# Kernel tuning notes

Measured on AMD Instinct MI355X. Metric: run time of the kernel, lower is better.

The kernel has to match this reference:

```python
import jax, jax.numpy as jnp
import numpy as np
from jax.scipy.special import digamma, gammaln

NUM_CLASSES = 3
FOCAL_GAMMA = 2.0
LABEL_SMOOTHING = 0.1
EVIDENTIAL_W = 0.1
CONTRASTIVE_W = 0.1
BOUNDARY_W = 0.15
TRIPLET_W = 0.1
QUALITY_W = 0.1
TRIPLET_MARGIN = 1.5


def setup_inputs() -> dict:
    key = jax.random.key(0)
    k1, k2, k3 = jax.random.split(key, 3)
    B, D = 4096, 512
    logits = jax.random.normal(k1, (B, NUM_CLASSES), dtype=jnp.float32)
    targets = jax.random.randint(k2, (B,), 0, 3)
    features = jax.random.normal(k3, (B, D), dtype=jnp.float32)
    alpha = jax.random.uniform(jax.random.fold_in(key, 7), (B, NUM_CLASSES), dtype=jnp.float32)
    focal_alpha = jnp.array([1.0, 2.0, 1.5], dtype=jnp.float32)
    class_weights = jnp.array([1.0, 2.0, 1.5], dtype=jnp.float32)
    return {"logits": logits, "targets": targets, "features": features,
            "alpha": alpha, "epoch": 1, "focal_alpha": focal_alpha,
            "class_weights": class_weights}


def reference(logits, targets, features, alpha, epoch, focal_alpha, class_weights):
    B = logits.shape[0]
    C = NUM_CLASSES

    # ---- focal loss (label-smoothed CE, torch semantics) ----
    logp = jax.nn.log_softmax(logits, axis=1)                      # [B,C]
    nll = -jnp.take_along_axis(logp, targets[:, None], axis=1)[:, 0]
    ce_ls = (1.0 - LABEL_SMOOTHING) * nll + LABEL_SMOOTHING * (-logp.mean(axis=1))
    pt = jnp.exp(-ce_ls)
    focal = (focal_alpha[targets] * (1.0 - pt) ** FOCAL_GAMMA * ce_ls).mean()

    # ---- weighted CE (torch weighted mean: sum(w*nll)/sum(w)) ----
    w = class_weights[targets]
    ce = (w * nll).sum() / w.sum()

    # ---- enhanced boundary loss ----
    probs = jax.nn.softmax(logits, axis=1)
    real = targets == 0
    semi = targets == 1
    syn = targets == 2
    rb = jnp.where(real, probs[:, 1] + 0.6 * probs[:, 2], 0.0).sum()
    sb = jnp.where(syn, probs[:, 1] + 0.4 * probs[:, 0], 0.0).sum()
    mb = jnp.where(semi, 1.0 - probs[:, 1] + 0.3 * (probs[:, 0] + probs[:, 2]), 0.0).sum()
    boundary = (rb + sb + 4.5 * mb) / (B + 1e-8)

    total = 0.4 * focal + 0.3 * ce + BOUNDARY_W * boundary

    # ---- normalized features and pairwise cosine-sim matrix ----
    norms = jnp.linalg.norm(features, axis=1, keepdims=True)
    f = features / jnp.maximum(norms, 1e-12)
    sim = f @ f.T                                                  # [B,B]
    same = targets[:, None] == targets[None, :]
    eye = jnp.eye(B, dtype=bool)

    # ---- enhanced contrastive loss ----
    pos = jnp.where(same, (1.0 - sim) ** 2, 0.0).sum()
    neg = jnp.where(~same, jnp.clip(sim - 0.2, 0.0) ** 2, 0.0).sum()
    semi_pair = semi[:, None] & semi[None, :]
    semi_l = jnp.where(semi_pair, (1.0 - sim) ** 2, 0.0).sum()
    contrastive = (pos + neg + 4.0 * semi_l) / (B * B + 1e-8)

    # ---- enhanced triplet loss (batch-hard, vectorized) ----
    d2 = jnp.clip(2.0 - 2.0 * sim, 0.0)
    dist = jnp.sqrt(jnp.where(eye, 1.0, d2))  # diag masked; safe sqrt
    pos_mask = same & ~eye
    neg_mask = ~same
    hp = jnp.max(jnp.where(pos_mask, dist, -jnp.inf), axis=1)
    hn = jnp.min(jnp.where(neg_mask, dist, jnp.inf), axis=1)
    valid = pos_mask.any(axis=1) & neg_mask.any(axis=1)
    margin = TRIPLET_MARGIN * jnp.where(targets == 1, 2.5, 1.0)
    tl = jax.nn.relu(hp - hn + margin)
    cnt = valid.sum()
    triplet = jnp.where(cnt > 0,
                        jnp.where(valid, tl, 0.0).sum() / jnp.maximum(cnt, 1),
                        0.0)

    # ---- quality-invariant loss (upper-tri same-class pairs) ----
    upper = jnp.triu(jnp.ones((B, B), dtype=bool), k=1)
    qmask = same & upper
    npairs = qmask.sum()
    q = jnp.where(qmask, (1.0 - sim) ** 2, 0.0).sum() / jnp.maximum(npairs, 1)
    frac2 = syn.astype(jnp.float32).mean()
    q = q * jnp.where(syn.sum() > 0, 1.0 + 2.5 * frac2, 1.0)
    quality = jnp.where(npairs > 0, q, 0.0)

    # ---- evidential loss ----
    onehot = jax.nn.one_hot(targets, C, dtype=jnp.float32)
    S = alpha.sum(axis=1, keepdims=True) + 1e-8
    likelihood = (onehot * (digamma(S) - digamma(alpha + 1e-8))).sum(axis=1)
    at = onehot + (1.0 - onehot) * alpha
    ats = at.sum(axis=1) + 1e-8
    kl = (gammaln(ats) - gammaln(at + 1e-8).sum(axis=1)
          + ((at - 1.0) * (digamma(at + 1e-8) - digamma(ats[:, None] + 1e-8))).sum(axis=1))
    annealing = min(1.0, (epoch / 25.0) ** 2)
    evidential = likelihood.mean() + annealing * 0.2 * kl.mean()

    total = (total + CONTRASTIVE_W * contrastive + TRIPLET_W * triplet
             + QUALITY_W * quality + EVIDENTIAL_W * evidential)
    return total
```

## Files before the change

kernel.cpp:

```cpp
#include <hip/hip_runtime.h>
#include <hip/hip_bf16.h>
#include <cstdint>

typedef __attribute__((ext_vector_type(8))) __bf16 bf8;
typedef __attribute__((ext_vector_type(4))) float f32x4;

#if defined(__has_builtin)
#if __has_builtin(__builtin_amdgcn_global_load_lds)
#define USE_GLL 1
#endif
#endif
#ifndef USE_GLL
#define USE_GLL 0
#endif

#if USE_GLL
__device__ __forceinline__ void gll16(const __bf16* g, __bf16* l){
  __builtin_amdgcn_global_load_lds(
      (const __attribute__((address_space(1))) void*)g,
      (__attribute__((address_space(3))) void*)l, 16, 0, 0);
}
#endif

__device__ __forceinline__ unsigned mapf(float x){
  unsigned u = __float_as_uint(x);
  return (u & 0x80000000u) ? ~u : (u | 0x80000000u);
}
__device__ __forceinline__ float unmapf(unsigned u){
  return __uint_as_float((u & 0x80000000u) ? (u & 0x7FFFFFFFu) : ~u);
}

__device__ float digammaf_(float x){
  float r = 0.f;
  while (x < 6.f){ r -= 1.f/x; x += 1.f; }
  float inv = 1.f/x, inv2 = inv*inv;
  r += logf(x) - 0.5f*inv
     - inv2*(0.08333333333f - inv2*(0.008333333333f - inv2*0.003968253968f));
  return r;
}

__global__ __launch_bounds__(256) void k_prep(const float* __restrict__ feat,
    __bf16* __restrict__ fb2,
    const float* __restrict__ logits, const int* __restrict__ targets,
    const float* __restrict__ alpha,  const float* __restrict__ fa,
    const float* __restrict__ cw, int B, int D,
    float* __restrict__ psum, unsigned* rowMinU, unsigned* rowMaxU){
  int bid = blockIdx.x, tid = threadIdx.x;
  int wave = tid >> 6, lane = tid & 63;

  int row = bid*4 + wave;
  const float* src = feat + (size_t)row*D;
  float ss = 0.f;
  for (int c = lane*4; c < D; c += 64*4){
    float4 v = *(const float4*)(src + c);
    ss += v.x*v.x + v.y*v.y + v.z*v.z + v.w*v.w;
  }
  #pragma unroll
  for (int off=32; off; off>>=1) ss += __shfl_xor(ss, off);
  float inv = 1.f / fmaxf(sqrtf(ss), 1e-12f);

  int p = row >> 6, r = row & 63;
  int rsw = (r >> 1) & 3;
  int NCH = D >> 5;
  for (int c = lane*8; c < D; c += 64*8){
    float4 v0 = *(const float4*)(src + c);
    float4 v1 = *(const float4*)(src + c + 4);
    bf8 o;
    o[0]=(__bf16)(v0.x*inv); o[1]=(__bf16)(v0.y*inv);
    o[2]=(__bf16)(v0.z*inv); o[3]=(__bf16)(v0.w*inv);
    o[4]=(__bf16)(v1.x*inv); o[5]=(__bf16)(v1.y*inv);
    o[6]=(__bf16)(v1.z*inv); o[7]=(__bf16)(v1.w*inv);
    int cc = c >> 5;
    int cb = (c >> 3) & 3;
    size_t off = (size_t)(p*NCH + cc)*2048 + r*32 + ((cb ^ rsw)*8);
    *(bf8*)(fb2 + off) = o;
  }

  if (tid < 4){ rowMinU[bid*4+tid] = 0xFFFFFFFFu; rowMaxU[bid*4+tid] = 0u; }

  if (wave == 0){
    float r0=0.f,r1=0.f,r2=0.f,r3=0.f,r4=0.f,r5=0.f;
    if (lane < 4){
      int i = bid*4 + lane;
      float l0=logits[3*i], l1=logits[3*i+1], l2=logits[3*i+2];
      int t = targets[i];
      float m = fmaxf(l0, fmaxf(l1,l2));
      float e0=expf(l0-m), e1=expf(l1-m), e2=expf(l2-m);
      float se = e0+e1+e2;
      float lse = m + logf(se);
      float lp0=l0-lse, lp1=l1-lse, lp2=l2-lse;
      float lpt = (t==0)?lp0:((t==1)?lp1:lp2);
      float nll = -lpt;
      float ce_ls = 0.9f*nll + 0.1f*(-(lp0+lp1+lp2)*(1.f/3.f));
      float pt = expf(-ce_ls);
      float om = 1.f - pt;
      float focal_i = fa[t]*om*om*ce_ls;
      float w = cw[t];
      float ce_n = w*nll, ce_d = w;
      float p0=e0/se, p1=e1/se, p2=e2/se;
      float bnd;
      if (t==0)      bnd = p1 + 0.6f*p2;
      else if (t==2) bnd = p1 + 0.4f*p0;
      else           bnd = 4.5f*(1.f - p1 + 0.3f*(p0+p2));
      float a0=alpha[3*i], a1=alpha[3*i+1], a2=alpha[3*i+2];
      float S = a0+a1+a2 + 1e-8f;
      float at_ = (t==0)?a0:((t==1)?a1:a2);
      float lik = digammaf_(S) - digammaf_(at_ + 1e-8f);
      float b0 = (t==0)?1.f:a0, b1 = (t==1)?1.f:a1, b2 = (t==2)?1.f:a2;
      float ats = b0+b1+b2 + 1e-8f;
      float psa = digammaf_(ats + 1e-8f);
      float kl = lgammaf(ats)
         - (lgammaf(b0+1e-8f)+lgammaf(b1+1e-8f)+lgammaf(b2+1e-8f))
         + (b0-1.f)*(digammaf_(b0+1e-8f)-psa)
         + (b1-1.f)*(digammaf_(b1+1e-8f)-psa)
         + (b2-1.f)*(digammaf_(b2+1e-8f)-psa);
      r0=focal_i; r1=ce_n; r2=ce_d; r3=bnd; r4=lik; r5=kl;
    }
    float s0 = ((__shfl(r0,0)+__shfl(r0,1))+__shfl(r0,2))+__shfl(r0,3);
    float s1 = ((__shfl(r1,0)+__shfl(r1,1))+__shfl(r1,2))+__shfl(r1,3);
    float s2 = ((__shfl(r2,0)+__shfl(r2,1))+__shfl(r2,2))+__shfl(r2,3);
    float s3 = ((__shfl(r3,0)+__shfl(r3,1))+__shfl(r3,2))+__shfl(r3,3);
    float s4 = ((__shfl(r4,0)+__shfl(r4,1))+__shfl(r4,2))+__shfl(r4,3);
    float s5 = ((__shfl(r5,0)+__shfl(r5,1))+__shfl(r5,2))+__shfl(r5,3);
    if (lane == 0){
      psum[bid*8+0]=s0; psum[bid*8+1]=s1; psum[bid*8+2]=s2;
      psum[bid*8+3]=s3; psum[bid*8+4]=s4; psum[bid*8+5]=s5;
    }
  }
}

__global__ __launch_bounds__(64) void k_pairs(const __bf16* __restrict__ fb2,
    const int* __restrict__ targets, int B, int D, int nblk,
    float* __restrict__ pairPart, unsigned* rowMinU, unsigned* rowMaxU){
  __shared__ __bf16 sA[2][2048];
  __shared__ __bf16 sB[2][2048];

  int raw = blockIdx.x;
  int q8 = nblk >> 3, r8 = nblk & 7;
  int xcd = raw & 7, o8 = raw >> 3;
  int t = (xcd < r8 ? xcd*(q8+1) : r8*(q8+1) + (xcd-r8)*q8) + o8;

  int bx = (int)((sqrtf(8.f*(float)t + 1.f) - 1.f)*0.5f);
  while ((bx+1)*(bx+2)/2 <= t) bx++;
  while (bx*(bx+1)/2 > t) bx--;
  int by = t - bx*(bx+1)/2;
  bool isDiag = (by == bx);
  int rowBase = by*64, colBase = bx*64;

  int lane = threadIdx.x;
  int quad = lane >> 4, l16 = lane & 15;
  int NCH = D/32;

  const __bf16* srcA = fb2 + (size_t)by*NCH*2048 + lane*8;
  const __bf16* srcB = fb2 + (size_t)bx*NCH*2048 + lane*8;
  const __bf16* sB0  = isDiag ? &sA[0][0] : &sB[0][0];

  int offA[4];
  #pragma unroll
  for (int mi=0; mi<4; mi++){
    int R = mi*16 + l16;
    offA[mi] = R*32 + ((quad ^ ((R>>1)&3))*8);
  }

  f32x4 C[4][4] = {};

#if USE_GLL
  #define STAGE(buf, it) do{ \
    const __bf16* ga_ = srcA + (it)*2048; \
    gll16(ga_ + 0*512, &sA[buf][0*512]); \
    gll16(ga_ + 1*512, &sA[buf][1*512]); \
    gll16(ga_ + 2*512, &sA[buf][2*512]); \
    gll16(ga_ + 3*512, &sA[buf][3*512]); \
    if (!isDiag){ \
      const __bf16* gb_ = srcB + (it)*2048; \
      gll16(gb_ + 0*512, &sB[buf][0*512]); \
      gll16(gb_ + 1*512, &sB[buf][1*512]); \
      gll16(gb_ + 2*512, &sB[buf][2*512]); \
      gll16(gb_ + 3*512, &sB[buf][3*512]); \
    } \
  }while(0)
#else
  #define STAGE(buf, it) do{ \
    const __bf16* ga_ = srcA + (it)*2048; \
    _Pragma("unroll") \
    for (int j=0; j<4; j++) \
      *(bf8*)&sA[buf][j*512 + lane*8] = *(const bf8*)(ga_ + j*512); \
    if (!isDiag){ \
      const __bf16* gb_ = srcB + (it)*2048; \
      _Pragma("unroll") \
      for (int j=0; j<4; j++) \
        *(bf8*)&sB[buf][j*512 + lane*8] = *(const bf8*)(gb_ + j*512); \
    } \
  }while(0)
#endif

  #define COMPUTE(buf) do{ \
    bf8 aF[4], bF[4]; \
    _Pragma("unroll") \
    for (int mi=0; mi<4; mi++) aF[mi] = *(const bf8*)(&sA[0][0] + (buf)*2048 + offA[mi]); \
    _Pragma("unroll") \
    for (int ni=0; ni<4; ni++) bF[ni] = *(const bf8*)(sB0 + (buf)*2048 + offA[ni]); \
    _Pragma("unroll") \
    for (int mi=0; mi<4; mi++) \
      _Pragma("unroll") \
      for (int ni=0; ni<4; ni++) \
        C[mi][ni] = __builtin_amdgcn_mfma_f32_16x16x32_bf16(aF[mi], bF[ni], C[mi][ni], 0,0,0); \
  }while(0)

  STAGE(0, 0);
  for (int it=0; it<NCH; it+=2){
    STAGE(1, it+1);
    COMPUTE(0);
    if (it+2 < NCH) STAGE(0, it+2);
    COMPUTE(1);
  }
  #undef STAGE
  #undef COMPUTE

  int tcol[4];
  #pragma unroll
  for (int ni=0; ni<4; ni++) tcol[ni] = targets[colBase + ni*16 + l16];

  float pos=0.f, neg=0.f, semi=0.f, diag=0.f;
  float cmin[4], cmax[4];
  #pragma unroll
  for (int ni=0; ni<4; ni++){ cmin[ni]=2.f; cmax[ni]=-2.f; }

  #pragma unroll
  for (int mi=0; mi<4; mi++){
    #pragma unroll
    for (int r=0; r<4; r++){
      int rl = mi*16 + quad*4 + r;
      int row = rowBase + rl;
      int tr = targets[row];
      float vmin = 2.f, vmax = -2.f;
      #pragma unroll
      for (int ni=0; ni<4; ni++){
        int col = colBase + ni*16 + l16;
        float s = C[mi][ni][r];
        if (tr == tcol[ni]){
          float omv = 1.f - s;
          float q = omv*omv;
          pos += q;
          if (tr == 1) semi += q;
          if (row == col) diag += q;
          else {
            vmin = fminf(vmin, s);
            cmin[ni] = fminf(cmin[ni], s);
          }
        } else {
          float c0 = fmaxf(s - 0.2f, 0.f);
          neg += c0*c0;
          vmax = fmaxf(vmax, s);
          cmax[ni] = fmaxf(cmax[ni], s);
        }
      }
      #pragma unroll
      for (int off=1; off<16; off<<=1){
        vmin = fminf(vmin, __shfl_xor(vmin, off));
        vmax = fmaxf(vmax, __shfl_xor(vmax, off));
      }
      if (l16 == 0){
        atomicMin(&rowMinU[row], mapf(vmin));
        atomicMax(&rowMaxU[row], mapf(vmax));
      }
    }
  }

  if (!isDiag){
    #pragma unroll
    for (int ni=0; ni<4; ni++){
      float cn = cmin[ni], cx = cmax[ni];
      cn = fminf(cn, __shfl_xor(cn, 16)); cn = fminf(cn, __shfl_xor(cn, 32));
      cx = fmaxf(cx, __shfl_xor(cx, 16)); cx = fmaxf(cx, __shfl_xor(cx, 32));
      if (quad == 0){
        int col = colBase + ni*16 + l16;
        atomicMin(&rowMinU[col], mapf(cn));
        atomicMax(&rowMaxU[col], mapf(cx));
      }
    }
  }

  #pragma unroll
  for (int off=32; off; off>>=1){
    pos  += __shfl_xor(pos, off);
    neg  += __shfl_xor(neg, off);
    semi += __shfl_xor(semi, off);
    diag += __shfl_xor(diag, off);
  }
  if (lane == 0){
    float fac = isDiag ? 1.f : 2.f;
    pairPart[t*4+0] = pos*fac;
    pairPart[t*4+1] = neg*fac;
    pairPart[t*4+2] = semi*fac;
    pairPart[t*4+3] = diag;
  }
}

__global__ __launch_bounds__(1024) void k_final(const int* __restrict__ targets,
    const int* __restrict__ epoch_p, int B, int nprep, int nblk,
    const float* __restrict__ pairPart, const float* __restrict__ psum,
    const unsigned* rowMinU, const unsigned* rowMaxU, float* out){
  int tid = threadIdx.x, wave = tid>>6, lane = tid&63;
  __shared__ float redf[16][8];
  __shared__ int   redi[16][4];
  __shared__ float tot6[6];
  __shared__ int   cns[3];
  __shared__ float ptot[4];

  {
    int c0=0,c1=0,c2=0;
    for (int i4 = tid; i4 < B/4; i4 += 1024){
      int4 tv = ((const int4*)targets)[i4];
      c0 += (tv.x==0)+(tv.y==0)+(tv.z==0)+(tv.w==0);
      c1 += (tv.x==1)+(tv.y==1)+(tv.z==1)+(tv.w==1);
      c2 += (tv.x==2)+(tv.y==2)+(tv.z==2)+(tv.w==2);
    }
    #pragma unroll
    for (int off=32; off; off>>=1){
      c0+=__shfl_xor(c0,off); c1+=__shfl_xor(c1,off); c2+=__shfl_xor(c2,off);
    }
    if (lane==0){ redi[wave][0]=c0; redi[wave][1]=c1; redi[wave][2]=c2; }
  }
  {
    float v0=0,v1=0,v2=0,v3=0,v4=0,v5=0;
    for (int s = tid; s < nprep; s += 1024){
      float4 a = *(const float4*)(psum + s*8);
      float4 b = *(const float4*)(psum + s*8 + 4);
      v0+=a.x; v1+=a.y; v2+=a.z; v3+=a.w; v4+=b.x; v5+=b.y;
    }
    #pragma unroll
    for (int off=32; off; off>>=1){
      v0+=__shfl_xor(v0,off); v1+=__shfl_xor(v1,off); v2+=__shfl_xor(v2,off);
      v3+=__shfl_xor(v3,off); v4+=__shfl_xor(v4,off); v5+=__shfl_xor(v5,off);
    }
    if (lane==0){
      redf[wave][0]=v0; redf[wave][1]=v1; redf[wave][2]=v2;
      redf[wave][3]=v3; redf[wave][4]=v4; redf[wave][5]=v5;
    }
  }
  __syncthreads();
  if (tid == 0){
    int c0=0,c1=0,c2=0;
    float v[6]={0,0,0,0,0,0};
    for (int w2=0; w2<16; w2++){
      c0+=redi[w2][0]; c1+=redi[w2][1]; c2+=redi[w2][2];
      for (int j=0;j<6;j++) v[j]+=redf[w2][j];
    }
    cns[0]=c0; cns[1]=c1; cns[2]=c2;
    for (int j=0;j<6;j++) tot6[j]=v[j];
  }
  __syncthreads();

  {
    float p=0,n=0,s2=0,d=0;
    for (int s = tid; s < nblk; s += 1024){
      float4 a = *(const float4*)(pairPart + s*4);
      p+=a.x; n+=a.y; s2+=a.z; d+=a.w;
    }
    #pragma unroll
    for (int off=32; off; off>>=1){
      p+=__shfl_xor(p,off); n+=__shfl_xor(n,off);
      s2+=__shfl_xor(s2,off); d+=__shfl_xor(d,off);
    }
    if (lane==0){ redf[wave][0]=p; redf[wave][1]=n; redf[wave][2]=s2; redf[wave][3]=d; }
  }
  __syncthreads();
  if (tid == 0){
    float a=0,b=0,c=0,e=0;
    for (int w2=0; w2<16; w2++){ a+=redf[w2][0]; b+=redf[w2][1]; c+=redf[w2][2]; e+=redf[w2][3]; }
    ptot[0]=a; ptot[1]=b; ptot[2]=c; ptot[3]=e;
  }
  __syncthreads();

  int n0=cns[0], n1=cns[1], n2=cns[2];

  float tsum = 0.f, tcnt = 0.f;
  for (int i = tid; i < B; i += 1024){
    int t = targets[i];
    int nt = (t==0)?n0:((t==1)?n1:n2);
    if (nt - 1 > 0 && B - nt > 0){
      float mn = unmapf(rowMinU[i]);
      float mx = unmapf(rowMaxU[i]);
      float hp = sqrtf(fmaxf(2.f - 2.f*mn, 0.f));
      float hn = sqrtf(fmaxf(2.f - 2.f*mx, 0.f));
      float margin = 1.5f * ((t==1) ? 2.5f : 1.f);
      float tl = fmaxf(hp - hn + margin, 0.f);
      tsum += tl; tcnt += 1.f;
    }
  }
  #pragma unroll
  for (int off=32; off; off>>=1){ tsum += __shfl_xor(tsum, off); tcnt += __shfl_xor(tcnt, off); }
  if (lane==0){ redf[wave][6]=tsum; redf[wave][7]=tcnt; }
  __syncthreads();

  if (tid==0){
    float ts=0, tn=0;
    for (int w2=0; w2<16; w2++){ ts+=redf[w2][6]; tn+=redf[w2][7]; }
    float triplet = (tn > 0.f) ? ts / fmaxf(tn, 1.f) : 0.f;
    float pos=ptot[0], neg=ptot[1], semi=ptot[2], diag=ptot[3];
    float Bf = (float)B;
    float focal = tot6[0] / Bf;
    float ce = tot6[1] / tot6[2];
    float boundary = tot6[3] / (Bf + 1e-8f);
    float contrastive = (pos + neg + 4.f*semi) / (Bf*Bf + 1e-8f);
    long long npl = ((long long)n0*(n0-1) + (long long)n1*(n1-1) + (long long)n2*(n2-1))/2;
    float qsum = (pos - diag) * 0.5f;
    float q = qsum / (float)(npl > 0 ? npl : 1);
    if (n2 > 0) q *= (1.f + 2.5f * ((float)n2 / Bf));
    float quality = (npl > 0) ? q : 0.f;
    int ep = epoch_p[0];
    float er = (float)ep / 25.f;
    float ann = fminf(1.f, er*er);
    float evidential = tot6[4]/Bf + ann*0.2f*tot6[5]/Bf;
    float total = 0.4f*focal + 0.3f*ce + 0.15f*boundary
                + 0.1f*contrastive + 0.1f*triplet + 0.1f*quality + 0.1f*evidential;
    out[0] = total;
  }
}

extern "C" void kernel_launch(void* const* d_in, const int* in_sizes, int n_in,
                              void* d_out, int out_size, void* d_ws, size_t ws_size,
                              hipStream_t stream){
  const float* logits   = (const float*)d_in[0];
  const int*   targets  = (const int*)d_in[1];
  const float* features = (const float*)d_in[2];
  const float* alpha    = (const float*)d_in[3];
  const int*   epoch    = (const int*)d_in[4];
  const float* fa       = (const float*)d_in[5];
  const float* cw       = (const float*)d_in[6];
  int B = in_sizes[1];
  int D = in_sizes[2] / B;
  int nprep = B/4;
  int T  = B / 64;
  int nblk = T*(T+1)/2;

  char* ws = (char*)d_ws;
  float*    psum     = (float*)(ws);
  float*    pairPart = (float*)(ws + 65536);
  unsigned* rowMinU  = (unsigned*)(ws + 131072);
  unsigned* rowMaxU  = (unsigned*)(ws + 131072 + (size_t)B*4);
  __bf16*   fb2      = (__bf16*)(ws + 131072 + (size_t)B*8);

  k_prep <<<nprep, 256, 0, stream>>>(features, fb2, logits, targets, alpha, fa, cw,
                                     B, D, psum, rowMinU, rowMaxU);
  k_pairs<<<nblk, 64, 0, stream>>>(fb2, targets, B, D, nblk, pairPart,
                                   rowMinU, rowMaxU);
  k_final<<<1, 1024, 0, stream>>>(targets, epoch, B, nprep, nblk, pairPart, psum,
                                  rowMinU, rowMaxU, (float*)d_out);
}
```

Before: 123.3 us.

## Enlarge pair tiles to 128x128 with four cooperating waves sharing LDS

The pairwise similarity kernel now uses 256-thread blocks covering 128x128 tiles. Each of the four waves computes a 64x64 sub-tile, and all waves cooperatively stage shared A/B panels into LDS. This cuts global traffic per MFMA and reduces the block count. The prep kernel's packed bf16 layout is changed to 128-row panels to match. The cost is block-wide barriers in the double-buffered loop, removal of the XCD-aware block remap, and fewer, larger blocks, which may hurt load balance.

```diff
diff --git a/kernel.cpp b/kernel.cpp
--- a/kernel.cpp
+++ b/kernel.cpp
@@ -59,7 +59,7 @@
   for (int off=32; off; off>>=1) ss += __shfl_xor(ss, off);
   float inv = 1.f / fmaxf(sqrtf(ss), 1e-12f);
 
-  int p = row >> 6, r = row & 63;
+  int p = row >> 7, r = row & 127;
   int rsw = (r >> 1) & 3;
   int NCH = D >> 5;
   for (int c = lane*8; c < D; c += 64*8){
@@ -72,7 +72,7 @@
     o[6]=(__bf16)(v1.z*inv); o[7]=(__bf16)(v1.w*inv);
     int cc = c >> 5;
     int cb = (c >> 3) & 3;
-    size_t off = (size_t)(p*NCH + cc)*2048 + r*32 + ((cb ^ rsw)*8);
+    size_t off = (size_t)(p*NCH + cc)*4096 + r*32 + ((cb ^ rsw)*8);
     *(bf8*)(fb2 + off) = o;
   }
 
@@ -129,67 +129,61 @@
   }
 }
 
-__global__ __launch_bounds__(64) void k_pairs(const __bf16* __restrict__ fb2,
-    const int* __restrict__ targets, int B, int D, int nblk,
+__global__ __launch_bounds__(256) void k_pairs(const __bf16* __restrict__ fb2,
+    const int* __restrict__ targets, int B, int D,
     float* __restrict__ pairPart, unsigned* rowMinU, unsigned* rowMaxU){
-  __shared__ __bf16 sA[2][2048];
-  __shared__ __bf16 sB[2][2048];
-
-  int raw = blockIdx.x;
-  int q8 = nblk >> 3, r8 = nblk & 7;
-  int xcd = raw & 7, o8 = raw >> 3;
-  int t = (xcd < r8 ? xcd*(q8+1) : r8*(q8+1) + (xcd-r8)*q8) + o8;
-
+  __shared__ __bf16 sA[2][4096];
+  __shared__ __bf16 sB[2][4096];
+
+  int t = blockIdx.x;
   int bx = (int)((sqrtf(8.f*(float)t + 1.f) - 1.f)*0.5f);
   while ((bx+1)*(bx+2)/2 <= t) bx++;
   while (bx*(bx+1)/2 > t) bx--;
   int by = t - bx*(bx+1)/2;
   bool isDiag = (by == bx);
-  int rowBase = by*64, colBase = bx*64;
-
-  int lane = threadIdx.x;
+
+  int tid = threadIdx.x;
+  int wave = tid >> 6, lane = tid & 63;
+  int wr = wave >> 1, wc = wave & 1;
   int quad = lane >> 4, l16 = lane & 15;
-  int NCH = D/32;
-
-  const __bf16* srcA = fb2 + (size_t)by*NCH*2048 + lane*8;
-  const __bf16* srcB = fb2 + (size_t)bx*NCH*2048 + lane*8;
+  int NCH = D >> 5;
+
+  int rowBase = by*128 + wr*64, colBase = bx*128 + wc*64;
+
+  int woff = wave*1024;
+  const __bf16* srcA = fb2 + (size_t)by*NCH*4096 + woff + lane*8;
+  const __bf16* srcB = fb2 + (size_t)bx*NCH*4096 + woff + lane*8;
   const __bf16* sB0  = isDiag ? &sA[0][0] : &sB[0][0];
 
-  int offA[4];
+  int offA[4], offB[4];
   #pragma unroll
   for (int mi=0; mi<4; mi++){
-    int R = mi*16 + l16;
-    offA[mi] = R*32 + ((quad ^ ((R>>1)&3))*8);
+    int RA = wr*64 + mi*16 + l16;
+    offA[mi] = RA*32 + ((quad ^ ((RA>>1)&3))*8);
+    int RB = wc*64 + mi*16 + l16;
+    offB[mi] = RB*32 + ((quad ^ ((RB>>1)&3))*8);
   }
 
   f32x4 C[4][4] = {};
 
 #if USE_GLL
   #define STAGE(buf, it) do{ \
-    const __bf16* ga_ = srcA + (it)*2048; \
-    gll16(ga_ + 0*512, &sA[buf][0*512]); \
-    gll16(ga_ + 1*512, &sA[buf][1*512]); \
-    gll16(ga_ + 2*512, &sA[buf][2*512]); \
-    gll16(ga_ + 3*512, &sA[buf][3*512]); \
+    gll16(srcA + (it)*4096 + 0*512, &sA[buf][woff + 0*512]); \
+    gll16(srcA + (it)*4096 + 1*512, &sA[buf][woff + 1*512]); \
     if (!isDiag){ \
-      const __bf16* gb_ = srcB + (it)*2048; \
-      gll16(gb_ + 0*512, &sB[buf][0*512]); \
-      gll16(gb_ + 1*512, &sB[buf][1*512]); \
-      gll16(gb_ + 2*512, &sB[buf][2*512]); \
-      gll16(gb_ + 3*512, &sB[buf][3*512]); \
+      gll16(srcB + (it)*4096 + 0*512, &sB[buf][woff + 0*512]); \
+      gll16(srcB + (it)*4096 + 1*512, &sB[buf][woff + 1*512]); \
     } \
   }while(0)
 #else
   #define STAGE(buf, it) do{ \
-    const __bf16* ga_ = srcA + (it)*2048; \
     _Pragma("unroll") \
-    for (int j=0; j<4; j++) \
-      *(bf8*)&sA[buf][j*512 + lane*8] = *(const bf8*)(ga_ + j*512); \
+    for (int j=0; j<2; j++) \
+      *(bf8*)&sA[buf][woff + j*512 + lane*8] = *(const bf8*)(srcA + (it)*4096 + j*512); \
     if (!isDiag){ \
-      const __bf16* gb_ = srcB + (it)*2048; \
       _Pragma("unroll") \
-      for (int j=0; j<4; j++) \
-        *(bf8*)&sB[buf][j*512 + lane*8] = *(const bf8*)(gb_ + j*512); \
+      for (int j=0; j<2; j++) \
+        *(bf8*)&sB[buf][woff + j*512 + lane*8] = *(const bf8*)(srcB + (it)*4096 + j*512); \
     } \
   }while(0)
 #endif
@@ -197,9 +191,9 @@
   #define COMPUTE(buf) do{ \
     bf8 aF[4], bF[4]; \
     _Pragma("unroll") \
-    for (int mi=0; mi<4; mi++) aF[mi] = *(const bf8*)(&sA[0][0] + (buf)*2048 + offA[mi]); \
+    for (int mi=0; mi<4; mi++) aF[mi] = *(const bf8*)(&sA[0][0] + (buf)*4096 + offA[mi]); \
     _Pragma("unroll") \
-    for (int ni=0; ni<4; ni++) bF[ni] = *(const bf8*)(sB0 + (buf)*2048 + offA[ni]); \
+    for (int ni=0; ni<4; ni++) bF[ni] = *(const bf8*)(sB0 + (buf)*4096 + offB[ni]); \
     _Pragma("unroll") \
     for (int mi=0; mi<4; mi++) \
       _Pragma("unroll") \
@@ -208,11 +202,14 @@
   }while(0)
 
   STAGE(0, 0);
+  __syncthreads();
   for (int it=0; it<NCH; it+=2){
     STAGE(1, it+1);
     COMPUTE(0);
+    __syncthreads();
     if (it+2 < NCH) STAGE(0, it+2);
     COMPUTE(1);
+    __syncthreads();
   }
   #undef STAGE
   #undef COMPUTE
@@ -290,10 +287,8 @@
   }
   if (lane == 0){
     float fac = isDiag ? 1.f : 2.f;
-    pairPart[t*4+0] = pos*fac;
-    pairPart[t*4+1] = neg*fac;
-    pairPart[t*4+2] = semi*fac;
-    pairPart[t*4+3] = diag;
+    float* dst = pairPart + ((size_t)t*4 + wave)*4;
+    dst[0] = pos*fac; dst[1] = neg*fac; dst[2] = semi*fac; dst[3] = diag;
   }
 }
 
@@ -432,8 +427,9 @@
   int B = in_sizes[1];
   int D = in_sizes[2] / B;
   int nprep = B/4;
-  int T  = B / 64;
+  int T  = B / 128;
   int nblk = T*(T+1)/2;
+  int nslot = nblk*4;
 
   char* ws = (char*)d_ws;
   float*    psum     = (float*)(ws);
@@ -444,8 +440,8 @@
 
   k_prep <<<nprep, 256, 0, stream>>>(features, fb2, logits, targets, alpha, fa, cw,
                                      B, D, psum, rowMinU, rowMaxU);
-  k_pairs<<<nblk, 64, 0, stream>>>(fb2, targets, B, D, nblk, pairPart,
-                                   rowMinU, rowMaxU);
-  k_final<<<1, 1024, 0, stream>>>(targets, epoch, B, nprep, nblk, pairPart, psum,
+  k_pairs<<<nblk, 256, 0, stream>>>(fb2, targets, B, D, pairPart,
+                                    rowMinU, rowMaxU);
+  k_final<<<1, 1024, 0, stream>>>(targets, epoch, B, nprep, nslot, pairPart, psum,
                                   rowMinU, rowMaxU, (float*)d_out);
 }
```

Measured after the change: 120.4 us. 2.3% less time.
